# Performance work log

Hardware: AMD Instinct MI355X
Metric: run time of the kernel (lower is better)

Reference implementation:

```python
import jax, jax.numpy as jnp
import numpy as np


def _dfb_filter():
    v = np.array([0.63, -0.193, 0.0972, -0.0526, 0.0272, -0.0144], dtype=np.float32)
    f = np.concatenate((v[::-1], v))
    f[::2] = -f[::2]
    return jnp.asarray(f)


def _resampm(x, type_, shift=1):
    # periodic shear along rows: out[..., i, j] = x[..., (i + k_j) % m, j]
    m, n = x.shape[-2], x.shape[-1]
    j = jnp.arange(n)
    k = (shift * j) % m if type_ == 1 else (-shift * j) % m
    rows = (jnp.arange(m)[:, None] + k[None, :]) % m  # [m, n]
    return x[..., rows, j[None, :]]


def _resamp(x, type_, shift=1):
    if type_ in (1, 2):
        return _resampm(x, type_, shift)
    return _resampm(x.swapaxes(-2, -1), type_ - 2, shift).swapaxes(-2, -1)


def _slice_1r(y):
    # interleave rows: [0, m, 1, m+1, ...]
    m = y.shape[-2] // 2
    a, b = y[..., :m, :], y[..., m:, :]
    return jnp.stack([a, b], axis=-2).reshape(y.shape)


def _slice_2c(y):
    # interleave cols: [0, n, 1, n+1, ...]
    n = y.shape[-1] // 2
    a, b = y[..., :n], y[..., n:]
    return jnp.stack([a, b], axis=-1).reshape(y.shape)


def _extend2(x, ru, rd, cl, cr, extmod):
    rx, cx = x.shape[-2], x.shape[-1]
    if extmod == 'per':
        y = jnp.concatenate([x[..., rx - ru:, :], x, x[..., :rd, :]], axis=-2)
    elif extmod == 'qper_col':
        cx2 = cx // 2  # cx is even here
        xs = jnp.concatenate([x[..., cx2:], x[..., :cx2]], axis=-1)
        y = jnp.concatenate([xs[..., rx - ru:, :], x, xs[..., :rd, :]], axis=-2)
    else:
        raise ValueError(extmod)
    return jnp.concatenate([y[..., cx - cl:], y, y[..., :cr]], axis=-1)


def _sep_conv(y, f):
    # depthwise separable filtering (torch used a dense diagonal kernel -> identical math)
    L = f.shape[0]
    ch = y.shape[1]
    dn = ('NCHW', 'OIHW', 'NCHW')
    kh = jnp.broadcast_to(f.reshape(1, 1, L, 1), (ch, 1, L, 1))
    y = jax.lax.conv_general_dilated(y, kh, (1, 1), 'VALID', dimension_numbers=dn, feature_group_count=ch)
    kw = jnp.broadcast_to(f.reshape(1, 1, 1, L), (ch, 1, 1, L))
    return jax.lax.conv_general_dilated(y, kw, (1, 1), 'VALID', dimension_numbers=dn, feature_group_count=ch)


def _sefilter2(x, f, extmod='per', shift=(0, 0)):
    L = f.shape[0]
    lf = (L - 1) / 2  # 5.5 for the 12-tap filter
    ru = int(np.floor(lf)) + shift[0]
    rd = int(np.ceil(lf)) - shift[0]
    cl = int(np.floor(lf)) + shift[1]
    cr = int(np.ceil(lf)) - shift[1]
    y = _extend2(x, ru, rd, cl, cr, extmod)
    return _sep_conv(y, f)


def _qprec(p0, p1, type2):
    if type2 == '1r':
        a = _resamp(p0, 4)
        b = jnp.roll(_resamp(p1, 4), 1, axis=-1)
        y = _slice_1r(jnp.concatenate([a, b], axis=-2))
        return _resamp(y, 1)
    elif type2 == '2c':
        a = _resamp(p0, 2)
        b = jnp.roll(_resamp(p1, 2), 1, axis=-2)
        y = _slice_2c(jnp.concatenate([a, b], axis=-1))
        return _resamp(y, 3)
    raise ValueError(type2)


def _fbrec(y0, y1, f, type2, extmod):
    p1 = -(2.0 ** -0.5) * (y1 + _sefilter2(y0, f, extmod))
    p0 = (2.0 ** 0.5) * y0 + _sefilter2(p1, f, extmod, (1, 1))
    return _qprec(p0, p1, type2)


def _dfbrec4(y0, y1, y2, y3):
    # dfbrec_layer for n=2 (4 directional subbands):
    # list reorder y[2:] = y[-1:1:-1] -> [y0, y1, y3, y2]; rebacksamp is a no-op for n=2.
    f = _dfb_filter()
    C = y0.shape[1]
    # new_fbrec_layer([y[1], y[3]], [y[0], y[2]], f, 'q', '2c', 'per')  (channel-batched)
    Y0 = jnp.concatenate([y1, y2], axis=1)
    Y1 = jnp.concatenate([y0, y3], axis=1)
    x = _fbrec(Y0, Y1, f, '2c', 'per')  # [N, 2C, H, 2W]
    x0, x1 = x[:, :C], x[:, C:]
    # fbrec_layer(x0, x1, f, 'q', '1r', 'qper_col')  -> [N, C, 2H, 2W]
    return _fbrec(x0, x1, f, '1r', 'qper_col')


def setup_inputs() -> dict:
    key = jax.random.key(0)
    ks = jax.random.split(key, 4)
    shp = (8, 32, 128, 128)
    return {('y%d' % i): jax.random.normal(ks[i], shp, dtype=jnp.float32) for i in range(4)}


def reference(y0, y1, y2, y3):
    return _dfbrec4(y0, y1, y2, y3)
```

## Files before the change

### kernel.cpp

```cpp
#include <hip/hip_runtime.h>

namespace {

constexpr float FF[12] = {0.0144f, 0.0272f, 0.0526f, 0.0972f, 0.193f, 0.63f,
                          -0.63f, -0.193f, -0.0972f, -0.0526f, -0.0272f, -0.0144f};
constexpr float SQ2   = 1.41421356237309515f;
constexpr float NISQ2 = -0.70710678118654752f;

template <int O, int W4>
__device__ __forceinline__ float4 hconv(const float4* R4, int row4, int j4) {
  float r[20];
#pragma unroll
  for (int d = 0; d < 5; ++d) {
    float4 t = R4[row4 + ((j4 + d - 2) & (W4 - 1))];
    r[4 * d + 0] = t.x; r[4 * d + 1] = t.y; r[4 * d + 2] = t.z; r[4 * d + 3] = t.w;
  }
  float4 o = make_float4(0.f, 0.f, 0.f, 0.f);
#pragma unroll
  for (int a = 0; a < 12; ++a) {
    const float fa = FF[a];
    o.x += fa * r[8 + 0 + a - O];
    o.y += fa * r[8 + 1 + a - O];
    o.z += fa * r[8 + 2 + a - O];
    o.w += fa * r[8 + 3 + a - O];
  }
  return o;
}

template <int O>
__device__ __forceinline__ float4 vconv_s1(const float4* S4, int i, int j4) {
  float4 o = make_float4(0.f, 0.f, 0.f, 0.f);
#pragma unroll
  for (int a = 0; a < 12; ++a) {
    const float fa = FF[a];
    float4 v = S4[((i + a - O) & 127) * 32 + j4];
    o.x += fa * v.x; o.y += fa * v.y; o.z += fa * v.z; o.w += fa * v.w;
  }
  return o;
}

template <int O>
__device__ __forceinline__ float4 vconv_s2(const float4* S4, int i, int j4) {
  float4 o = make_float4(0.f, 0.f, 0.f, 0.f);
#pragma unroll
  for (int a = 0; a < 12; ++a) {
    const float fa = FF[a];
    int r = i + a - O;
    int idx = ((unsigned)r < 128u) ? (r * 64 + j4) : ((r & 127) * 64 + (j4 ^ 32));
    float4 v = S4[idx];
    o.x += fa * v.x; o.y += fa * v.y; o.z += fa * v.z; o.w += fa * v.w;
  }
  return o;
}

}

__global__ __launch_bounds__(1024) void s1_kernel(
    const float* __restrict__ y0, const float* __restrict__ y1,
    const float* __restrict__ y2, const float* __restrict__ y3,
    float* __restrict__ xout) {
  __shared__ float bufA[16384];
  __shared__ float bufB[16384];
  float4* A4 = reinterpret_cast<float4*>(bufA);
  float4* B4 = reinterpret_cast<float4*>(bufB);

  const int p  = blockIdx.x;
  const int b  = p >> 6;
  const int cc = p & 63;
  const int sub = (b * 32 + (cc & 31)) << 14;
  const float* Y0 = (cc < 32 ? y1 : y2) + sub;
  const float* Y1 = (cc < 32 ? y0 : y3) + sub;
  const float4* Y04 = reinterpret_cast<const float4*>(Y0);
  const float4* Y14 = reinterpret_cast<const float4*>(Y1);
  float* xp = xout + (size_t)p * 32768;

  const int tid = threadIdx.x;

#pragma unroll
  for (int k = 0; k < 4; ++k) A4[tid + k * 1024] = Y04[tid + k * 1024];
  __syncthreads();

#pragma unroll
  for (int k = 0; k < 4; ++k) {
    int g = tid + k * 1024;
    B4[g] = vconv_s1<5>(A4, g >> 5, g & 31);
  }
  __syncthreads();

#pragma unroll
  for (int k = 0; k < 4; ++k) {
    int g = tid + k * 1024;
    int i = g >> 5, j4 = g & 31;
    float4 h = hconv<5, 32>(B4, i * 32, j4);
    float4 yv = Y14[g];
    float4 o;
    o.x = NISQ2 * (yv.x + h.x);
    o.y = NISQ2 * (yv.y + h.y);
    o.z = NISQ2 * (yv.z + h.z);
    o.w = NISQ2 * (yv.w + h.w);
    A4[g] = o;
  }
  __syncthreads();

#pragma unroll
  for (int k = 0; k < 4; ++k) {
    int g = tid + k * 1024;
    B4[g] = vconv_s1<6>(A4, g >> 5, g & 31);
  }
  __syncthreads();

  float4 pv[4];
#pragma unroll
  for (int k = 0; k < 4; ++k) {
    int g = tid + k * 1024;
    int i = g >> 5, j4 = g & 31;
    float4 h = hconv<6, 32>(B4, i * 32, j4);
    float4 yv = Y04[g];
    pv[k].x = SQ2 * yv.x + h.x;
    pv[k].y = SQ2 * yv.y + h.y;
    pv[k].z = SQ2 * yv.z + h.z;
    pv[k].w = SQ2 * yv.w + h.w;
  }
  __syncthreads();
#pragma unroll
  for (int k = 0; k < 4; ++k) B4[tid + k * 1024] = pv[k];
  __syncthreads();

#pragma unroll
  for (int k = 0; k < 8; ++k) {
    int t = tid + k * 1024;
    int i = t >> 6;
    int j4b = (t & 63) << 2;
    float tmp[4];
#pragma unroll
    for (int m = 0; m < 4; ++m) {
      int jo = j4b + m;
      int J = (i + jo) & 255;
      int c = J >> 1;
      float v;
      if (J & 1) {
        int r = (i - 1 - c) & 127;
        v = bufA[r * 128 + c];
      } else {
        int r = (i - c) & 127;
        v = bufB[r * 128 + c];
      }
      tmp[m] = v;
    }
    reinterpret_cast<float4*>(xp)[t] = make_float4(tmp[0], tmp[1], tmp[2], tmp[3]);
  }
}

__global__ __launch_bounds__(1024) void s2_kernel(const float* __restrict__ x,
                                                  float* __restrict__ out) {
  __shared__ float buf[32768];
  float4* X4 = reinterpret_cast<float4*>(buf);

  const int q = blockIdx.x;
  const int b = q >> 5, c = q & 31;
  const float* x0 = x + (size_t)(b * 64 + c) * 32768;
  const float* x1 = x + (size_t)(b * 64 + 32 + c) * 32768;
  const float4* x04 = reinterpret_cast<const float4*>(x0);
  const float4* x14 = reinterpret_cast<const float4*>(x1);
  float* op = out + (size_t)q * 65536;

  const int tid = threadIdx.x;
  float4 tv[8];

#pragma unroll
  for (int k = 0; k < 8; ++k) X4[tid + k * 1024] = x04[tid + k * 1024];
  __syncthreads();

#pragma unroll
  for (int k = 0; k < 8; ++k) {
    int g = tid + k * 1024;
    tv[k] = vconv_s2<5>(X4, g >> 6, g & 63);
  }
  __syncthreads();
#pragma unroll
  for (int k = 0; k < 8; ++k) X4[tid + k * 1024] = tv[k];
  __syncthreads();

#pragma unroll
  for (int k = 0; k < 8; ++k) {
    int g = tid + k * 1024;
    int i = g >> 6, j4 = g & 63;
    float4 h = hconv<5, 64>(X4, i * 64, j4);
    float4 xv = x14[g];
    tv[k].x = NISQ2 * (xv.x + h.x);
    tv[k].y = NISQ2 * (xv.y + h.y);
    tv[k].z = NISQ2 * (xv.z + h.z);
    tv[k].w = NISQ2 * (xv.w + h.w);
  }
  __syncthreads();
#pragma unroll
  for (int k = 0; k < 8; ++k) X4[tid + k * 1024] = tv[k];
  __syncthreads();

#pragma unroll
  for (int k = 0; k < 32; ++k) {
    int t = tid + k * 1024;
    int i = t >> 7;
    int u = t & 127;
    int jo = (u << 1) | ((i + 1) & 1);
    int r = ((i + jo) & 255) >> 1;
    int cc2 = (jo - 1 - r) & 255;
    op[i * 256 + jo] = buf[r * 256 + cc2];
  }

#pragma unroll
  for (int k = 0; k < 8; ++k) {
    int g = tid + k * 1024;
    tv[k] = vconv_s2<6>(X4, g >> 6, g & 63);
  }
  __syncthreads();
#pragma unroll
  for (int k = 0; k < 8; ++k) X4[tid + k * 1024] = tv[k];
  __syncthreads();

#pragma unroll
  for (int k = 0; k < 8; ++k) {
    int g = tid + k * 1024;
    int i = g >> 6, j4 = g & 63;
    float4 h = hconv<6, 64>(X4, i * 64, j4);
    float4 xv = x04[g];
    tv[k].x = SQ2 * xv.x + h.x;
    tv[k].y = SQ2 * xv.y + h.y;
    tv[k].z = SQ2 * xv.z + h.z;
    tv[k].w = SQ2 * xv.w + h.w;
  }
  __syncthreads();
#pragma unroll
  for (int k = 0; k < 8; ++k) X4[tid + k * 1024] = tv[k];
  __syncthreads();

#pragma unroll
  for (int k = 0; k < 32; ++k) {
    int t = tid + k * 1024;
    int i = t >> 7;
    int u = t & 127;
    int jo = (u << 1) | (i & 1);
    int r = ((i + jo) & 255) >> 1;
    int cc2 = (jo - r) & 255;
    op[i * 256 + jo] = buf[r * 256 + cc2];
  }
}

extern "C" void kernel_launch(void* const* d_in, const int* in_sizes, int n_in,
                              void* d_out, int out_size, void* d_ws, size_t ws_size,
                              hipStream_t stream) {
  const float* y0 = (const float*)d_in[0];
  const float* y1 = (const float*)d_in[1];
  const float* y2 = (const float*)d_in[2];
  const float* y3 = (const float*)d_in[3];
  float* xws = (float*)d_ws;
  float* outp = (float*)d_out;

  s1_kernel<<<512, 1024, 0, stream>>>(y0, y1, y2, y3, xws);
  s2_kernel<<<256, 1024, 0, stream>>>(xws, outp);
}
```

Before: 196.7 us.

## Fuse both reconstruction stages into one kernel keeping intermediates in registers

Merges the two kernels into one: each block computes both first-stage planes for a channel, keeps the results in registers, then runs the second stage without writing the intermediate to global workspace. The second stage's output writes become float4 vector stores, with half the elements buffered in registers across the two sub-steps. This removes the workspace round-trip and one launch. In exchange the grid shrinks from 512 to 256 blocks and register pressure rises considerably (xv0, xv1, ov arrays), which may cause spills or lower occupancy.

```diff
diff --git a/kernel.cpp b/kernel.cpp
--- a/kernel.cpp
+++ b/kernel.cpp
@@ -53,28 +53,13 @@
   return o;
 }
 
-}
-
-__global__ __launch_bounds__(1024) void s1_kernel(
-    const float* __restrict__ y0, const float* __restrict__ y1,
-    const float* __restrict__ y2, const float* __restrict__ y3,
-    float* __restrict__ xout) {
-  __shared__ float bufA[16384];
-  __shared__ float bufB[16384];
+__device__ __forceinline__ void s1_plane(const float4* __restrict__ Y04,
+                                         const float4* __restrict__ Y14,
+                                         float* __restrict__ bufA,
+                                         float* __restrict__ bufB,
+                                         float4* __restrict__ xv, int tid) {
   float4* A4 = reinterpret_cast<float4*>(bufA);
   float4* B4 = reinterpret_cast<float4*>(bufB);
-
-  const int p  = blockIdx.x;
-  const int b  = p >> 6;
-  const int cc = p & 63;
-  const int sub = (b * 32 + (cc & 31)) << 14;
-  const float* Y0 = (cc < 32 ? y1 : y2) + sub;
-  const float* Y1 = (cc < 32 ? y0 : y3) + sub;
-  const float4* Y04 = reinterpret_cast<const float4*>(Y0);
-  const float4* Y14 = reinterpret_cast<const float4*>(Y1);
-  float* xp = xout + (size_t)p * 32768;
-
-  const int tid = threadIdx.x;
 
 #pragma unroll
   for (int k = 0; k < 4; ++k) A4[tid + k * 1024] = Y04[tid + k * 1024];
@@ -93,12 +78,8 @@
     int i = g >> 5, j4 = g & 31;
     float4 h = hconv<5, 32>(B4, i * 32, j4);
     float4 yv = Y14[g];
-    float4 o;
-    o.x = NISQ2 * (yv.x + h.x);
-    o.y = NISQ2 * (yv.y + h.y);
-    o.z = NISQ2 * (yv.z + h.z);
-    o.w = NISQ2 * (yv.w + h.w);
-    A4[g] = o;
+    A4[g] = make_float4(NISQ2 * (yv.x + h.x), NISQ2 * (yv.y + h.y),
+                        NISQ2 * (yv.z + h.z), NISQ2 * (yv.w + h.w));
   }
   __syncthreads();
 
@@ -116,10 +97,8 @@
     int i = g >> 5, j4 = g & 31;
     float4 h = hconv<6, 32>(B4, i * 32, j4);
     float4 yv = Y04[g];
-    pv[k].x = SQ2 * yv.x + h.x;
-    pv[k].y = SQ2 * yv.y + h.y;
-    pv[k].z = SQ2 * yv.z + h.z;
-    pv[k].w = SQ2 * yv.w + h.w;
+    pv[k] = make_float4(SQ2 * yv.x + h.x, SQ2 * yv.y + h.y,
+                        SQ2 * yv.z + h.z, SQ2 * yv.w + h.w);
   }
   __syncthreads();
 #pragma unroll
@@ -130,47 +109,50 @@
   for (int k = 0; k < 8; ++k) {
     int t = tid + k * 1024;
     int i = t >> 6;
-    int j4b = (t & 63) << 2;
+    int jb = (t & 63) << 2;
     float tmp[4];
 #pragma unroll
     for (int m = 0; m < 4; ++m) {
-      int jo = j4b + m;
+      int jo = jb + m;
       int J = (i + jo) & 255;
       int c = J >> 1;
-      float v;
-      if (J & 1) {
-        int r = (i - 1 - c) & 127;
-        v = bufA[r * 128 + c];
-      } else {
-        int r = (i - c) & 127;
-        v = bufB[r * 128 + c];
-      }
-      tmp[m] = v;
+      tmp[m] = (J & 1) ? bufA[((i - 1 - c) & 127) * 128 + c]
+                       : bufB[((i - c) & 127) * 128 + c];
     }
-    reinterpret_cast<float4*>(xp)[t] = make_float4(tmp[0], tmp[1], tmp[2], tmp[3]);
-  }
-}
-
-__global__ __launch_bounds__(1024) void s2_kernel(const float* __restrict__ x,
-                                                  float* __restrict__ out) {
+    xv[k] = make_float4(tmp[0], tmp[1], tmp[2], tmp[3]);
+  }
+  __syncthreads();
+}
+
+}
+
+__global__ __launch_bounds__(1024) void fused_kernel(
+    const float* __restrict__ y0, const float* __restrict__ y1,
+    const float* __restrict__ y2, const float* __restrict__ y3,
+    float* __restrict__ out) {
   __shared__ float buf[32768];
+  float* bufA = buf;
+  float* bufB = buf + 16384;
   float4* X4 = reinterpret_cast<float4*>(buf);
 
   const int q = blockIdx.x;
-  const int b = q >> 5, c = q & 31;
-  const float* x0 = x + (size_t)(b * 64 + c) * 32768;
-  const float* x1 = x + (size_t)(b * 64 + 32 + c) * 32768;
-  const float4* x04 = reinterpret_cast<const float4*>(x0);
-  const float4* x14 = reinterpret_cast<const float4*>(x1);
-  float* op = out + (size_t)q * 65536;
-
   const int tid = threadIdx.x;
+  const size_t sub4 = (size_t)q * 4096;
+
+  const float4* Y0a = reinterpret_cast<const float4*>(y2) + sub4;
+  const float4* Y1a = reinterpret_cast<const float4*>(y3) + sub4;
+  const float4* Y0b = reinterpret_cast<const float4*>(y1) + sub4;
+  const float4* Y1b = reinterpret_cast<const float4*>(y0) + sub4;
+
+  float4 xv1[8], xv0[8];
+  s1_plane(Y0a, Y1a, bufA, bufB, xv1, tid);
+  s1_plane(Y0b, Y1b, bufA, bufB, xv0, tid);
+
+#pragma unroll
+  for (int k = 0; k < 8; ++k) X4[tid + k * 1024] = xv0[k];
+  __syncthreads();
+
   float4 tv[8];
-
-#pragma unroll
-  for (int k = 0; k < 8; ++k) X4[tid + k * 1024] = x04[tid + k * 1024];
-  __syncthreads();
-
 #pragma unroll
   for (int k = 0; k < 8; ++k) {
     int g = tid + k * 1024;
@@ -186,26 +168,28 @@
     int g = tid + k * 1024;
     int i = g >> 6, j4 = g & 63;
     float4 h = hconv<5, 64>(X4, i * 64, j4);
-    float4 xv = x14[g];
-    tv[k].x = NISQ2 * (xv.x + h.x);
-    tv[k].y = NISQ2 * (xv.y + h.y);
-    tv[k].z = NISQ2 * (xv.z + h.z);
-    tv[k].w = NISQ2 * (xv.w + h.w);
-  }
-  __syncthreads();
-#pragma unroll
-  for (int k = 0; k < 8; ++k) X4[tid + k * 1024] = tv[k];
-  __syncthreads();
-
-#pragma unroll
-  for (int k = 0; k < 32; ++k) {
+    xv1[k] = make_float4(NISQ2 * (xv1[k].x + h.x), NISQ2 * (xv1[k].y + h.y),
+                         NISQ2 * (xv1[k].z + h.z), NISQ2 * (xv1[k].w + h.w));
+  }
+  __syncthreads();
+#pragma unroll
+  for (int k = 0; k < 8; ++k) X4[tid + k * 1024] = xv1[k];
+  __syncthreads();
+
+  float ov[32];
+#pragma unroll
+  for (int k = 0; k < 16; ++k) {
     int t = tid + k * 1024;
-    int i = t >> 7;
-    int u = t & 127;
-    int jo = (u << 1) | ((i + 1) & 1);
-    int r = ((i + jo) & 255) >> 1;
-    int cc2 = (jo - 1 - r) & 255;
-    op[i * 256 + jo] = buf[r * 256 + cc2];
+    int i = t >> 6;
+    int jb = (t & 63) << 2;
+    int m0 = 1 - (i & 1);
+#pragma unroll
+    for (int s = 0; s < 2; ++s) {
+      int jo = jb + m0 + 2 * s;
+      int r = ((i + jo) & 255) >> 1;
+      int cc2 = (jo - 1 - r) & 255;
+      ov[2 * k + s] = buf[r * 256 + cc2];
+    }
   }
 
 #pragma unroll
@@ -223,26 +207,39 @@
     int g = tid + k * 1024;
     int i = g >> 6, j4 = g & 63;
     float4 h = hconv<6, 64>(X4, i * 64, j4);
-    float4 xv = x04[g];
-    tv[k].x = SQ2 * xv.x + h.x;
-    tv[k].y = SQ2 * xv.y + h.y;
-    tv[k].z = SQ2 * xv.z + h.z;
-    tv[k].w = SQ2 * xv.w + h.w;
-  }
-  __syncthreads();
-#pragma unroll
-  for (int k = 0; k < 8; ++k) X4[tid + k * 1024] = tv[k];
-  __syncthreads();
-
-#pragma unroll
-  for (int k = 0; k < 32; ++k) {
+    xv0[k] = make_float4(SQ2 * xv0[k].x + h.x, SQ2 * xv0[k].y + h.y,
+                         SQ2 * xv0[k].z + h.z, SQ2 * xv0[k].w + h.w);
+  }
+  __syncthreads();
+#pragma unroll
+  for (int k = 0; k < 8; ++k) X4[tid + k * 1024] = xv0[k];
+  __syncthreads();
+
+  float4* op4 = reinterpret_cast<float4*>(out) + (size_t)q * 16384;
+#pragma unroll
+  for (int k = 0; k < 16; ++k) {
     int t = tid + k * 1024;
-    int i = t >> 7;
-    int u = t & 127;
-    int jo = (u << 1) | (i & 1);
-    int r = ((i + jo) & 255) >> 1;
-    int cc2 = (jo - r) & 255;
-    op[i * 256 + jo] = buf[r * 256 + cc2];
+    int i = t >> 6;
+    int jb = (t & 63) << 2;
+    float4 v;
+    if (i & 1) {
+      int jo1 = jb + 1, jo3 = jb + 3;
+      int r1 = ((i + jo1) & 255) >> 1;
+      int r3 = ((i + jo3) & 255) >> 1;
+      v.x = ov[2 * k];
+      v.y = buf[r1 * 256 + ((jo1 - r1) & 255)];
+      v.z = ov[2 * k + 1];
+      v.w = buf[r3 * 256 + ((jo3 - r3) & 255)];
+    } else {
+      int jo0 = jb, jo2 = jb + 2;
+      int r0 = ((i + jo0) & 255) >> 1;
+      int r2 = ((i + jo2) & 255) >> 1;
+      v.x = buf[r0 * 256 + ((jo0 - r0) & 255)];
+      v.y = ov[2 * k];
+      v.z = buf[r2 * 256 + ((jo2 - r2) & 255)];
+      v.w = ov[2 * k + 1];
+    }
+    op4[t] = v;
   }
 }
 
@@ -253,9 +250,8 @@
   const float* y1 = (const float*)d_in[1];
   const float* y2 = (const float*)d_in[2];
   const float* y3 = (const float*)d_in[3];
-  float* xws = (float*)d_ws;
   float* outp = (float*)d_out;
-
-  s1_kernel<<<512, 1024, 0, stream>>>(y0, y1, y2, y3, xws);
-  s2_kernel<<<256, 1024, 0, stream>>>(xws, outp);
-}
+  (void)d_ws; (void)ws_size;
+
+  fused_kernel<<<256, 1024, 0, stream>>>(y0, y1, y2, y3, outp);
+}
```

Measured after the change: 218.5 us. 11.1% more time.
